# Kernel tuning notes

Hardware: AMD Instinct MI355X
Metric: run time of the kernel (lower is better)

## Reference

```python
import jax, jax.numpy as jnp
import numpy as np

B, N, QD = 2, 4096, 1024
CD = 1024
H, DH = 8, 64
INNER = H * DH  # 512


def setup_inputs() -> dict:
    key = jax.random.key(0)
    ks = jax.random.split(key, 10)
    s = lambda d: (1.0 / np.sqrt(d)).astype(np.float32)
    return {
        "x": jax.random.normal(ks[0], (B, N, QD), dtype=jnp.float32),
        "context": jax.random.normal(ks[1], (B, N, CD), dtype=jnp.float32),
        "mask": jax.random.randint(ks[2], (B, N + 1), 0, 2) > 0,
        # weights stored as [in, out] (y = x @ W), matching torch Linear math
        "Wq": jax.random.normal(ks[3], (QD, INNER), dtype=jnp.float32) * s(QD),
        "Wk": jax.random.normal(ks[4], (CD, INNER), dtype=jnp.float32) * s(CD),
        "Wv": jax.random.normal(ks[5], (CD, INNER), dtype=jnp.float32) * s(CD),
        "Wk_bg": jax.random.normal(ks[6], (QD, INNER), dtype=jnp.float32) * s(QD),
        "Wv_bg": jax.random.normal(ks[7], (QD, INNER), dtype=jnp.float32) * s(QD),
        "Wout": jax.random.normal(ks[8], (INNER, QD), dtype=jnp.float32) * s(INNER),
        "b_out": jax.random.normal(ks[9], (QD,), dtype=jnp.float32) * 0.01,
    }


def reference(x, context, mask, Wq, Wk, Wv, Wk_bg, Wv_bg, Wout, b_out):
    b, n, _ = x.shape
    scale = DH ** -0.5

    q = x @ Wq                                             # [b, n, inner]
    pooled_x = jax.lax.stop_gradient(jnp.mean(x, axis=1, keepdims=True))  # [b, 1, qd]
    k = jnp.concatenate([context @ Wk, pooled_x @ Wk_bg], axis=1)  # [b, n+1, inner]
    v = jnp.concatenate([context @ Wv, pooled_x @ Wv_bg], axis=1)  # [b, n+1, inner]

    split = lambda t: t.reshape(b, t.shape[1], H, DH).transpose(0, 2, 1, 3)  # b h j d
    qh, kh, vh = split(q), split(k), split(v)

    sim = jnp.einsum('bhid,bhjd->bhij', qh, kh) * scale     # [b, h, n, n+1]
    neg = -jnp.finfo(sim.dtype).max
    sim = jnp.where(mask[:, None, None, :], sim, neg)
    attn = jax.nn.softmax(sim, axis=-1)
    out = jnp.einsum('bhij,bhjd->bhid', attn, vh)           # [b, h, n, d]
    out = out.transpose(0, 2, 1, 3).reshape(b, n, INNER)    # [b, n, inner]
    return out @ Wout + b_out                                # dropout p=0 -> identity
```

## Files before the change

### kernel.cpp

```cpp
#include <hip/hip_runtime.h>
#include <stdint.h>

#define N_TOK 4096
#define QDIM  1024
#define CDIM  1024
#define NH    8
#define DH    64
#define INNER 512
#define BATCH 2
#define N1    4097
#define N1P   4128
#define NJB   129
#define NJBP  132
#define VROWS 80
#define KTILE_SH 2048
#define VTILE_SH 2560

typedef __attribute__((ext_vector_type(8))) short short8;
typedef __attribute__((ext_vector_type(4))) float f32x4;
typedef __attribute__((ext_vector_type(4))) uint32_t u32x4;

__device__ __forceinline__ short f2bf(float f) {
    union { float f; uint32_t u; } x; x.f = f;
    uint32_t r = x.u + 0x7fffu + ((x.u >> 16) & 1u);
    return (short)(r >> 16);
}

__device__ __forceinline__ void async_copy16(void* lds, const void* g) {
    __builtin_amdgcn_global_load_lds(
        (const __attribute__((address_space(1))) void*)g,
        (__attribute__((address_space(3))) void*)lds, 16, 0, 0);
}

#define NB_CAST 16384
#define NB_TC   2048
#define NB_POOL 64
__global__ __launch_bounds__(256) void prep_kernel(
        const float* __restrict__ x, const float* __restrict__ ctx,
        const float* __restrict__ Wq, const float* __restrict__ Wk,
        const float* __restrict__ Wv, const float* __restrict__ Wout,
        short* __restrict__ x_bf, short* __restrict__ c_bf,
        short* __restrict__ Wqt, short* __restrict__ Wkvt, short* __restrict__ Wot,
        float* __restrict__ part, float scale_q) {
    __shared__ float tile[32][33];
    int blk = blockIdx.x, t = threadIdx.x;
    if (blk < NB_CAST) {
        const int n4 = BATCH * N_TOK * QDIM / 4;
        int i = blk * 256 + t;
        bool first = i < n4;
        const float* s = first ? x : ctx;
        short* d = first ? x_bf : c_bf;
        int j = first ? i : i - n4;
        float4 v = ((const float4*)s)[j];
        ((short4*)d)[j] = make_short4(f2bf(v.x), f2bf(v.y), f2bf(v.z), f2bf(v.w));
    } else if (blk < NB_CAST + NB_TC) {
        int rel = blk - NB_CAST;
        int z = rel >> 9, bid = rel & 511;
        const float* W; short* Wt; int K, N; float scale = 1.f;
        if (z == 0)      { W = Wq;   Wt = Wqt;  K = QDIM;  N = INNER; scale = scale_q; }
        else if (z == 1) { W = Wk;   Wt = Wkvt; K = CDIM;  N = INNER; }
        else if (z == 2) { W = Wv;   Wt = Wkvt + (size_t)INNER * CDIM; K = CDIM; N = INNER; }
        else             { W = Wout; Wt = Wot;  K = INNER; N = QDIM; }
        int ntn = N >> 5;
        int n0 = (bid & (ntn - 1)) * 32, k0 = (bid / ntn) * 32;
        int tx = t & 31, ty = t >> 5;
        for (int r = ty; r < 32; r += 8)
            tile[r][tx] = W[(size_t)(k0 + r) * N + n0 + tx];
        __syncthreads();
        for (int r = ty; r < 32; r += 8)
            Wt[(size_t)(n0 + r) * K + k0 + tx] = f2bf(tile[tx][r] * scale);
    } else {
        int rel = blk - NB_CAST - NB_TC;
        int c = rel & 31, b = rel >> 5;
        float s0 = 0.f, s1 = 0.f, s2 = 0.f, s3 = 0.f;
        const float* xp = x + ((size_t)b * N_TOK + c * 128) * QDIM;
        for (int n = 0; n < 128; n++) {
            const float* row = xp + (size_t)n * QDIM;
            s0 += row[t];
            s1 += row[256 + t];
            s2 += row[512 + t];
            s3 += row[768 + t];
        }
        float* pp = part + ((size_t)b * 32 + c) * QDIM;
        pp[t] = s0; pp[256 + t] = s1; pp[512 + t] = s2; pp[768 + t] = s3;
    }
}

__global__ __launch_bounds__(256) void transpose_v_kernel(
        const short* __restrict__ vin, short* __restrict__ vout,
        const int* __restrict__ mask) {
    __shared__ short tile[32][65];
    __shared__ int mloc[32];
    int bh = blockIdx.z, b = bh >> 3;
    int j0 = blockIdx.x * 32, jb = blockIdx.x;
    int tx = threadIdx.x & 63, ty = threadIdx.x >> 6;
    const short* src = vin + (size_t)bh * N1P * DH;
    if (j0 < N1P) {
        for (int r = ty; r < 32; r += 4)
            tile[r][tx] = src[(size_t)(j0 + r) * DH + tx];
    }
    if (threadIdx.x < 32) {
        int j = j0 + threadIdx.x;
        mloc[threadIdx.x] = (j < N1) ? mask[b * N1 + j] : 0;
    }
    __syncthreads();
    int tp = threadIdx.x & 31, dy = threadIdx.x >> 5;
    int s = (tp >> 3) * 4 + (tp & 3) + ((tp >> 2) & 1) * 16;
    bool mk = mloc[s] != 0;
    short* dst = vout + ((size_t)bh * NJBP + jb) * VTILE_SH;
    for (int d = dy; d < DH; d += 8) {
        int swz = (((tp >> 3) ^ ((d >> 1) & 3)) << 3) | (tp & 7);
        dst[d * 32 + swz] = mk ? tile[s][d] : (short)0;
    }
    if (dy == 0) dst[64 * 32 + tp] = mk ? (short)0x3F80 : (short)0;
    if (dy == 1)
        for (int d = 65; d < 80; d++) dst[d * 32 + tp] = 0;
}

__global__ __launch_bounds__(256) void qkv_gemm_kernel(
        const short* __restrict__ x_bf, const short* __restrict__ c_bf,
        const short* __restrict__ Wqt, const short* __restrict__ Wkvt,
        const float* __restrict__ part, const float* __restrict__ Wkbg,
        const float* __restrict__ Wvbg,
        short* __restrict__ q_bf, short* __restrict__ k_bf, short* __restrict__ v_tmp) {
    __shared__ short As[128 * 32];
    __shared__ short Bs[128 * 32];
    __shared__ float pooled[QDIM];
    const int t = threadIdx.x;
    int bid = (blockIdx.x & 7) * 97 + (blockIdx.x >> 3);

    if (bid >= 768) {
        int sub = bid - 768;
        int b = sub & 1, jb = sub >> 1;
        for (int d = t; d < QDIM; d += 256) {
            float s = 0.f;
            for (int c = 0; c < 32; c++) s += part[((size_t)b * 32 + c) * QDIM + d];
            pooled[d] = s * (1.f / (float)N_TOK);
        }
        __syncthreads();
        int flat = jb * 256 + t;
        int matv = flat >> 9;
        int o = flat & 511;
        const float* W = matv ? Wvbg : Wkbg;
        float s = 0.f;
        for (int k = 0; k < QDIM; k++) s += pooled[k] * W[(size_t)k * INNER + o];
        int h = o >> 6, d = o & 63;
        if (matv) {
            v_tmp[(((size_t)(b * NH + h)) * N1P + N_TOK) * DH + d] = f2bf(s);
        } else {
            k_bf[((size_t)(b * NH + h)) * NJBP * KTILE_SH + 128 * KTILE_SH
                 + (d >> 5) * 1024 + (d & 31)] = f2bf(s);
        }
        if (jb == 0) {
            for (int idx = t; idx < NH * 31 * DH; idx += 256) {
                int h2 = idx / (31 * DH);
                int r2 = idx % (31 * DH);
                int rr = 1 + r2 / DH;
                int d2 = r2 % DH;
                k_bf[((size_t)(b * NH + h2)) * NJBP * KTILE_SH + 128 * KTILE_SH
                     + (d2 >> 5) * 1024 + rr * 32 + (d2 & 31)] = 0;
            }
            for (int idx = t; idx < NH * 3 * KTILE_SH; idx += 256) {
                int h2 = idx / (3 * KTILE_SH);
                int r2 = idx % (3 * KTILE_SH);
                k_bf[((size_t)(b * NH + h2)) * NJBP * KTILE_SH + 129 * KTILE_SH + r2] = 0;
            }
        }
        return;
    }

    const int lane = t & 63, w = t >> 6;
    const int wr = w >> 1, wc = w & 1;
    const int lo = lane & 15, g = lane >> 4;
    const int arow = lane >> 2;
    const int ac8 = (lane & 3) * 8;

    const short *A, *W;
    int m0, n0, which;
    if (bid < 256) { A = x_bf; W = Wqt;  m0 = (bid >> 2) * 128; n0 = (bid & 3) * 128; which = 0; }
    else { int i = bid - 256; A = c_bf; W = Wkvt; m0 = (i >> 3) * 128; n0 = (i & 7) * 128;
           which = (n0 < 512) ? 1 : 2; }

    f32x4 acc[4][4] = {};
    for (int k0 = 0; k0 < 1024; k0 += 32) {
        for (int q = 0; q < 2; q++) {
            int seg = w * 2 + q;
            async_copy16(&As[seg * 512], A + (size_t)(m0 + seg * 16 + arow) * 1024 + k0 + ac8);
            async_copy16(&Bs[seg * 512], W + (size_t)(n0 + seg * 16 + arow) * 1024 + k0 + ac8);
        }
        __syncthreads();
        short8 af[4], bfv[4];
        #pragma unroll
        for (int i = 0; i < 4; i++)
            af[i] = *(const short8*)&As[(wr * 64 + i * 16 + lo) * 32 + g * 8];
        #pragma unroll
        for (int j = 0; j < 4; j++)
            bfv[j] = *(const short8*)&Bs[(wc * 64 + j * 16 + lo) * 32 + g * 8];
        #pragma unroll
        for (int i = 0; i < 4; i++)
            #pragma unroll
            for (int j = 0; j < 4; j++)
                acc[i][j] = __builtin_amdgcn_mfma_f32_16x16x32_bf16(af[i], bfv[j], acc[i][j], 0, 0, 0);
        __syncthreads();
    }

    if (which == 0) {
        #pragma unroll
        for (int i = 0; i < 4; i++)
            #pragma unroll
            for (int j = 0; j < 4; j++) {
                int row = m0 + wr * 64 + i * 16 + g * 4;
                int col0 = n0 + wc * 64 + j * 16 + lo;
                int h = col0 >> 6, d = col0 & 63;
                f32x4 v = acc[i][j];
                #pragma unroll
                for (int r = 0; r < 4; r++) {
                    int m = row + r;
                    int b = m >> 12, ii = m & 4095;
                    q_bf[(((size_t)(b * NH + h)) * N_TOK + ii) * DH + d] = f2bf(v[r]);
                }
            }
    } else if (which == 1) {
        #pragma unroll
        for (int i = 0; i < 4; i++)
            #pragma unroll
            for (int j = 0; j < 4; j++) {
                int row = m0 + wr * 64 + i * 16 + g * 4;
                int col0 = n0 + wc * 64 + j * 16 + lo;
                int h = col0 >> 6, d = col0 & 63;
                f32x4 v = acc[i][j];
                #pragma unroll
                for (int r = 0; r < 4; r++) {
                    int m = row + r;
                    int b = m >> 12, ii = m & 4095;
                    int off = (d >> 5) * 1024 + (ii & 31) * 32 + (d & 31);
                    off ^= ((ii >> 1) & 3) << 3;
                    k_bf[((size_t)(b * NH + h)) * NJBP * KTILE_SH + (ii >> 5) * KTILE_SH
                         + off] = f2bf(v[r]);
                }
            }
    } else {
        #pragma unroll
        for (int i = 0; i < 4; i++)
            #pragma unroll
            for (int j = 0; j < 4; j++) {
                int row = m0 + wr * 64 + i * 16 + g * 4;
                int col0 = n0 + wc * 64 + j * 16 + lo;
                int col = col0 - 512;
                int h = col >> 6, d = col & 63;
                f32x4 v = acc[i][j];
                #pragma unroll
                for (int r = 0; r < 4; r++) {
                    int m = row + r;
                    int b = m >> 12, ii = m & 4095;
                    v_tmp[(((size_t)(b * NH + h)) * N1P + ii) * DH + d] = f2bf(v[r]);
                }
            }
    }
}

__global__ __launch_bounds__(256) void out_gemm_kernel(
        const short* __restrict__ A, const short* __restrict__ Wt,
        float* __restrict__ outf, const float* __restrict__ bias) {
    __shared__ short As[128 * 32];
    __shared__ short Bs[128 * 32];
    const int t = threadIdx.x;
    const int lane = t & 63, w = t >> 6;
    const int wr = w >> 1, wc = w & 1;
    const int lo = lane & 15, g = lane >> 4;
    const int arow = lane >> 2;
    const int ac8 = (lane & 3) * 8;
    const int bid = (blockIdx.x & 7) * 64 + (blockIdx.x >> 3);
    const int m0 = (bid & 63) * 128, n0 = (bid >> 6) * 128;

    f32x4 acc[4][4] = {};
    for (int k0 = 0; k0 < INNER; k0 += 32) {
        for (int q = 0; q < 2; q++) {
            int seg = w * 2 + q;
            async_copy16(&As[seg * 512], A + (size_t)(m0 + seg * 16 + arow) * INNER + k0 + ac8);
            async_copy16(&Bs[seg * 512], Wt + (size_t)(n0 + seg * 16 + arow) * INNER + k0 + ac8);
        }
        __syncthreads();
        short8 af[4], bfv[4];
        #pragma unroll
        for (int i = 0; i < 4; i++)
            af[i] = *(const short8*)&As[(wr * 64 + i * 16 + lo) * 32 + g * 8];
        #pragma unroll
        for (int j = 0; j < 4; j++)
            bfv[j] = *(const short8*)&Bs[(wc * 64 + j * 16 + lo) * 32 + g * 8];
        #pragma unroll
        for (int i = 0; i < 4; i++)
            #pragma unroll
            for (int j = 0; j < 4; j++)
                acc[i][j] = __builtin_amdgcn_mfma_f32_16x16x32_bf16(af[i], bfv[j], acc[i][j], 0, 0, 0);
        __syncthreads();
    }
    #pragma unroll
    for (int i = 0; i < 4; i++)
        #pragma unroll
        for (int j = 0; j < 4; j++) {
            int row = m0 + wr * 64 + i * 16 + g * 4;
            int col = n0 + wc * 64 + j * 16 + lo;
            f32x4 v = acc[i][j];
            #pragma unroll
            for (int r = 0; r < 4; r++)
                outf[(size_t)(row + r) * QDIM + col] = v[r] + bias[col];
        }
}

__global__ __launch_bounds__(256, 2) void attn_kernel(
        const short* __restrict__ qb,
        const short* __restrict__ kb,
        const short* __restrict__ vtb,
        short* __restrict__ ob) {
    const int t = threadIdx.x, lane = t & 63, w = t >> 6;
    const int lo = lane & 15, g = lane >> 4;
    const int gs = g ^ ((lo >> 1) & 3);
    const int id = blockIdx.x;
    const int h = id & 7, b = (id >> 3) & 1, qt = id >> 4;
    const int q0 = qt * 128 + w * 32;
    const size_t bh = (size_t)(b * NH + h);

    const short* qp = qb + (bh * N_TOK + q0 + lo) * DH;
    short8 qa[2][2];
    qa[0][0] = *(const short8*)(qp + g * 8);
    qa[0][1] = *(const short8*)(qp + 32 + g * 8);
    qa[1][0] = *(const short8*)(qp + 16 * DH + g * 8);
    qa[1][1] = *(const short8*)(qp + 16 * DH + 32 + g * 8);

    __shared__ short Kl[2][4][KTILE_SH];
    __shared__ short Vl[2][4][VTILE_SH];

    const short* ksrc = kb + bh * (size_t)NJBP * KTILE_SH + w * 512 + lane * 8;
    const short* vsrc = vtb + bh * (size_t)NJBP * VTILE_SH + w * 512 + lane * 8;

    f32x4 o[2][5] = {};
    f32x4 z = {};

    #pragma unroll
    for (int s = 0; s < 4; s++) {
        async_copy16(&Kl[0][s][w * 512], ksrc + (size_t)s * KTILE_SH);
        async_copy16(&Vl[0][s][w * 512], vsrc + (size_t)s * VTILE_SH);
        if (w == 0) async_copy16(&Vl[0][s][2048], vsrc + (size_t)s * VTILE_SH + 2048);
    }
    __syncthreads();

    for (int it = 0; it < 33; ++it) {
        const int cur = it & 1;
        if (it < 32) {
            const short* ks = ksrc + (size_t)(4 * it + 4) * KTILE_SH;
            const short* vs = vsrc + (size_t)(4 * it + 4) * VTILE_SH;
            #pragma unroll
            for (int s = 0; s < 4; s++) {
                async_copy16(&Kl[cur ^ 1][s][w * 512], ks + (size_t)s * KTILE_SH);
                async_copy16(&Vl[cur ^ 1][s][w * 512], vs + (size_t)s * VTILE_SH);
                if (w == 0) async_copy16(&Vl[cur ^ 1][s][2048], vs + (size_t)s * VTILE_SH + 2048);
            }
        }
        #pragma unroll
        for (int sub = 0; sub < 4; ++sub) {
            const short* kl = &Kl[cur][sub][0];
            const short* vl = &Vl[cur][sub][0];
            __builtin_amdgcn_s_setprio(1);
            short8 kf00 = *(const short8*)&kl[(lo) * 32 + gs * 8];
            short8 kf01 = *(const short8*)&kl[1024 + (lo) * 32 + gs * 8];
            short8 kf10 = *(const short8*)&kl[(16 + lo) * 32 + gs * 8];
            short8 kf11 = *(const short8*)&kl[1024 + (16 + lo) * 32 + gs * 8];
            short8 vfr[5];
            #pragma unroll
            for (int f = 0; f < 5; f++)
                vfr[f] = *(const short8*)&vl[(f * 16 + lo) * 32 + gs * 8];
            #pragma unroll
            for (int rg = 0; rg < 2; rg++) {
                f32x4 s0 = __builtin_amdgcn_mfma_f32_16x16x32_bf16(kf00, qa[rg][0], z, 0, 0, 0);
                s0 = __builtin_amdgcn_mfma_f32_16x16x32_bf16(kf01, qa[rg][1], s0, 0, 0, 0);
                f32x4 s1 = __builtin_amdgcn_mfma_f32_16x16x32_bf16(kf10, qa[rg][0], z, 0, 0, 0);
                s1 = __builtin_amdgcn_mfma_f32_16x16x32_bf16(kf11, qa[rg][1], s1, 0, 0, 0);
                uint32_t u0 = __float_as_uint(__builtin_amdgcn_exp2f(s0[0])) + 0x8000u;
                uint32_t u1 = __float_as_uint(__builtin_amdgcn_exp2f(s0[1])) + 0x8000u;
                uint32_t u2 = __float_as_uint(__builtin_amdgcn_exp2f(s0[2])) + 0x8000u;
                uint32_t u3 = __float_as_uint(__builtin_amdgcn_exp2f(s0[3])) + 0x8000u;
                uint32_t u4 = __float_as_uint(__builtin_amdgcn_exp2f(s1[0])) + 0x8000u;
                uint32_t u5 = __float_as_uint(__builtin_amdgcn_exp2f(s1[1])) + 0x8000u;
                uint32_t u6 = __float_as_uint(__builtin_amdgcn_exp2f(s1[2])) + 0x8000u;
                uint32_t u7 = __float_as_uint(__builtin_amdgcn_exp2f(s1[3])) + 0x8000u;
                u32x4 pr;
                pr[0] = __builtin_amdgcn_perm(u1, u0, 0x07060302u);
                pr[1] = __builtin_amdgcn_perm(u3, u2, 0x07060302u);
                pr[2] = __builtin_amdgcn_perm(u5, u4, 0x07060302u);
                pr[3] = __builtin_amdgcn_perm(u7, u6, 0x07060302u);
                short8 pa = __builtin_bit_cast(short8, pr);
                #pragma unroll
                for (int f = 0; f < 5; f++)
                    o[rg][f] = __builtin_amdgcn_mfma_f32_16x16x32_bf16(pa, vfr[f], o[rg][f], 0, 0, 0);
            }
            __builtin_amdgcn_s_setprio(0);
        }
        __syncthreads();
    }

    short* op = ob + ((size_t)(b * N_TOK) + q0) * INNER + h * DH;
    #pragma unroll
    for (int rg = 0; rg < 2; rg++)
        #pragma unroll
        for (int r = 0; r < 4; r++) {
            float l = __shfl(o[rg][4][r], lane & 48);
            float inv = (l > 0.f) ? 1.f / l : 0.f;
            short* o_ = op + (size_t)(rg * 16 + g * 4 + r) * INNER;
            o_[lo]      = f2bf(o[rg][0][r] * inv);
            o_[16 + lo] = f2bf(o[rg][1][r] * inv);
            o_[32 + lo] = f2bf(o[rg][2][r] * inv);
            o_[48 + lo] = f2bf(o[rg][3][r] * inv);
        }
}

extern "C" void kernel_launch(void* const* d_in, const int* in_sizes, int n_in,
                              void* d_out, int out_size, void* d_ws, size_t ws_size,
                              hipStream_t stream) {
    const float* x    = (const float*)d_in[0];
    const float* ctx  = (const float*)d_in[1];
    const int*   mask = (const int*)d_in[2];
    const float* Wq   = (const float*)d_in[3];
    const float* Wk   = (const float*)d_in[4];
    const float* Wv   = (const float*)d_in[5];
    const float* Wkbg = (const float*)d_in[6];
    const float* Wvbg = (const float*)d_in[7];
    const float* Wout = (const float*)d_in[8];
    const float* bout = (const float*)d_in[9];
    float* out = (float*)d_out;

    char* p = (char*)d_ws;
    auto alloc = [&](size_t b) { char* r = p; p += (b + 255) & ~(size_t)255; return r; };
    short* x_bf  = (short*)alloc((size_t)BATCH * N_TOK * QDIM * 2);
    short* c_bf  = (short*)alloc((size_t)BATCH * N_TOK * CDIM * 2);
    short* Wqt   = (short*)alloc((size_t)INNER * QDIM * 2);
    short* Wkvt  = (short*)alloc((size_t)2 * INNER * CDIM * 2);
    short* Wot   = (short*)alloc((size_t)QDIM * INNER * 2);
    short* q_bf  = (short*)alloc((size_t)BATCH * NH * N_TOK * DH * 2);
    short* k_bf  = (short*)alloc((size_t)BATCH * NH * NJBP * KTILE_SH * 2);
    short* v_tmp = (short*)alloc((size_t)BATCH * NH * N1P * DH * 2);
    short* vt_bf = (short*)alloc((size_t)BATCH * NH * NJBP * VTILE_SH * 2);
    short* o_bf  = (short*)alloc((size_t)BATCH * N_TOK * INNER * 2);
    float* part  = (float*)alloc((size_t)BATCH * 32 * QDIM * 4);

    const float SCALE_Q = 0.125f * 1.4426950408889634f;

    prep_kernel<<<NB_CAST + NB_TC + NB_POOL, 256, 0, stream>>>(
        x, ctx, Wq, Wk, Wv, Wout, x_bf, c_bf, Wqt, Wkvt, Wot, part, SCALE_Q);

    qkv_gemm_kernel<<<776, 256, 0, stream>>>(
        x_bf, c_bf, Wqt, Wkvt, part, Wkbg, Wvbg, q_bf, k_bf, v_tmp);

    transpose_v_kernel<<<dim3(NJBP, 1, BATCH * NH), 256, 0, stream>>>(v_tmp, vt_bf, mask);

    attn_kernel<<<512, 256, 0, stream>>>(q_bf, k_bf, vt_bf, o_bf);

    out_gemm_kernel<<<512, 256, 0, stream>>>(o_bf, Wot, out, bout);
}
```

Baseline: 308.1 us.

## Halve attention query tile per block to double grid and raise occupancy

```diff
diff --git a/kernel.cpp b/kernel.cpp
--- a/kernel.cpp
+++ b/kernel.cpp
@@ -308,7 +308,7 @@
         }
 }
 
-__global__ __launch_bounds__(256, 2) void attn_kernel(
+__global__ __launch_bounds__(256, 4) void attn_kernel(
         const short* __restrict__ qb,
         const short* __restrict__ kb,
         const short* __restrict__ vtb,
@@ -318,47 +318,48 @@
     const int gs = g ^ ((lo >> 1) & 3);
     const int id = blockIdx.x;
     const int h = id & 7, b = (id >> 3) & 1, qt = id >> 4;
-    const int q0 = qt * 128 + w * 32;
+    const int q0 = qt * 64 + w * 16;
     const size_t bh = (size_t)(b * NH + h);
 
     const short* qp = qb + (bh * N_TOK + q0 + lo) * DH;
-    short8 qa[2][2];
-    qa[0][0] = *(const short8*)(qp + g * 8);
-    qa[0][1] = *(const short8*)(qp + 32 + g * 8);
-    qa[1][0] = *(const short8*)(qp + 16 * DH + g * 8);
-    qa[1][1] = *(const short8*)(qp + 16 * DH + 32 + g * 8);
-
-    __shared__ short Kl[2][4][KTILE_SH];
-    __shared__ short Vl[2][4][VTILE_SH];
+    short8 qa0 = *(const short8*)(qp + g * 8);
+    short8 qa1 = *(const short8*)(qp + 32 + g * 8);
+
+    __shared__ short Kl[2][2][KTILE_SH];
+    __shared__ short Vl[2][2][VTILE_SH];
 
     const short* ksrc = kb + bh * (size_t)NJBP * KTILE_SH + w * 512 + lane * 8;
     const short* vsrc = vtb + bh * (size_t)NJBP * VTILE_SH + w * 512 + lane * 8;
 
-    f32x4 o[2][5] = {};
+    f32x4 o[5] = {};
     f32x4 z = {};
 
-    #pragma unroll
-    for (int s = 0; s < 4; s++) {
-        async_copy16(&Kl[0][s][w * 512], ksrc + (size_t)s * KTILE_SH);
-        async_copy16(&Vl[0][s][w * 512], vsrc + (size_t)s * VTILE_SH);
-        if (w == 0) async_copy16(&Vl[0][s][2048], vsrc + (size_t)s * VTILE_SH + 2048);
+    async_copy16(&Kl[0][0][w * 512], ksrc);
+    async_copy16(&Vl[0][0][w * 512], vsrc);
+    async_copy16(&Kl[0][1][w * 512], ksrc + KTILE_SH);
+    async_copy16(&Vl[0][1][w * 512], vsrc + VTILE_SH);
+    if (w == 0) {
+        async_copy16(&Vl[0][0][2048], vsrc + 2048);
+        async_copy16(&Vl[0][1][2048], vsrc + VTILE_SH + 2048);
     }
     __syncthreads();
 
-    for (int it = 0; it < 33; ++it) {
+    for (int it = 0; it < 66; ++it) {
         const int cur = it & 1;
-        if (it < 32) {
-            const short* ks = ksrc + (size_t)(4 * it + 4) * KTILE_SH;
-            const short* vs = vsrc + (size_t)(4 * it + 4) * VTILE_SH;
-            #pragma unroll
-            for (int s = 0; s < 4; s++) {
-                async_copy16(&Kl[cur ^ 1][s][w * 512], ks + (size_t)s * KTILE_SH);
-                async_copy16(&Vl[cur ^ 1][s][w * 512], vs + (size_t)s * VTILE_SH);
-                if (w == 0) async_copy16(&Vl[cur ^ 1][s][2048], vs + (size_t)s * VTILE_SH + 2048);
-            }
-        }
-        #pragma unroll
-        for (int sub = 0; sub < 4; ++sub) {
+        if (it < 65) {
+            const short* ks = ksrc + (size_t)(2 * it + 2) * KTILE_SH;
+            const short* vs = vsrc + (size_t)(2 * it + 2) * VTILE_SH;
+            async_copy16(&Kl[cur ^ 1][0][w * 512], ks);
+            async_copy16(&Vl[cur ^ 1][0][w * 512], vs);
+            async_copy16(&Kl[cur ^ 1][1][w * 512], ks + KTILE_SH);
+            async_copy16(&Vl[cur ^ 1][1][w * 512], vs + VTILE_SH);
+            if (w == 0) {
+                async_copy16(&Vl[cur ^ 1][0][2048], vs + 2048);
+                async_copy16(&Vl[cur ^ 1][1][2048], vs + VTILE_SH + 2048);
+            }
+        }
+        #pragma unroll
+        for (int sub = 0; sub < 2; ++sub) {
             const short* kl = &Kl[cur][sub][0];
             const short* vl = &Vl[cur][sub][0];
             __builtin_amdgcn_s_setprio(1);
@@ -370,30 +371,27 @@
             #pragma unroll
             for (int f = 0; f < 5; f++)
                 vfr[f] = *(const short8*)&vl[(f * 16 + lo) * 32 + gs * 8];
-            #pragma unroll
-            for (int rg = 0; rg < 2; rg++) {
-                f32x4 s0 = __builtin_amdgcn_mfma_f32_16x16x32_bf16(kf00, qa[rg][0], z, 0, 0, 0);
-                s0 = __builtin_amdgcn_mfma_f32_16x16x32_bf16(kf01, qa[rg][1], s0, 0, 0, 0);
-                f32x4 s1 = __builtin_amdgcn_mfma_f32_16x16x32_bf16(kf10, qa[rg][0], z, 0, 0, 0);
-                s1 = __builtin_amdgcn_mfma_f32_16x16x32_bf16(kf11, qa[rg][1], s1, 0, 0, 0);
-                uint32_t u0 = __float_as_uint(__builtin_amdgcn_exp2f(s0[0])) + 0x8000u;
-                uint32_t u1 = __float_as_uint(__builtin_amdgcn_exp2f(s0[1])) + 0x8000u;
-                uint32_t u2 = __float_as_uint(__builtin_amdgcn_exp2f(s0[2])) + 0x8000u;
-                uint32_t u3 = __float_as_uint(__builtin_amdgcn_exp2f(s0[3])) + 0x8000u;
-                uint32_t u4 = __float_as_uint(__builtin_amdgcn_exp2f(s1[0])) + 0x8000u;
-                uint32_t u5 = __float_as_uint(__builtin_amdgcn_exp2f(s1[1])) + 0x8000u;
-                uint32_t u6 = __float_as_uint(__builtin_amdgcn_exp2f(s1[2])) + 0x8000u;
-                uint32_t u7 = __float_as_uint(__builtin_amdgcn_exp2f(s1[3])) + 0x8000u;
-                u32x4 pr;
-                pr[0] = __builtin_amdgcn_perm(u1, u0, 0x07060302u);
-                pr[1] = __builtin_amdgcn_perm(u3, u2, 0x07060302u);
-                pr[2] = __builtin_amdgcn_perm(u5, u4, 0x07060302u);
-                pr[3] = __builtin_amdgcn_perm(u7, u6, 0x07060302u);
-                short8 pa = __builtin_bit_cast(short8, pr);
-                #pragma unroll
-                for (int f = 0; f < 5; f++)
-                    o[rg][f] = __builtin_amdgcn_mfma_f32_16x16x32_bf16(pa, vfr[f], o[rg][f], 0, 0, 0);
-            }
+            f32x4 s0 = __builtin_amdgcn_mfma_f32_16x16x32_bf16(kf00, qa0, z, 0, 0, 0);
+            s0 = __builtin_amdgcn_mfma_f32_16x16x32_bf16(kf01, qa1, s0, 0, 0, 0);
+            f32x4 s1 = __builtin_amdgcn_mfma_f32_16x16x32_bf16(kf10, qa0, z, 0, 0, 0);
+            s1 = __builtin_amdgcn_mfma_f32_16x16x32_bf16(kf11, qa1, s1, 0, 0, 0);
+            uint32_t u0 = __float_as_uint(__builtin_amdgcn_exp2f(s0[0])) + 0x8000u;
+            uint32_t u1 = __float_as_uint(__builtin_amdgcn_exp2f(s0[1])) + 0x8000u;
+            uint32_t u2 = __float_as_uint(__builtin_amdgcn_exp2f(s0[2])) + 0x8000u;
+            uint32_t u3 = __float_as_uint(__builtin_amdgcn_exp2f(s0[3])) + 0x8000u;
+            uint32_t u4 = __float_as_uint(__builtin_amdgcn_exp2f(s1[0])) + 0x8000u;
+            uint32_t u5 = __float_as_uint(__builtin_amdgcn_exp2f(s1[1])) + 0x8000u;
+            uint32_t u6 = __float_as_uint(__builtin_amdgcn_exp2f(s1[2])) + 0x8000u;
+            uint32_t u7 = __float_as_uint(__builtin_amdgcn_exp2f(s1[3])) + 0x8000u;
+            u32x4 pr;
+            pr[0] = __builtin_amdgcn_perm(u1, u0, 0x07060302u);
+            pr[1] = __builtin_amdgcn_perm(u3, u2, 0x07060302u);
+            pr[2] = __builtin_amdgcn_perm(u5, u4, 0x07060302u);
+            pr[3] = __builtin_amdgcn_perm(u7, u6, 0x07060302u);
+            short8 pa = __builtin_bit_cast(short8, pr);
+            #pragma unroll
+            for (int f = 0; f < 5; f++)
+                o[f] = __builtin_amdgcn_mfma_f32_16x16x32_bf16(pa, vfr[f], o[f], 0, 0, 0);
             __builtin_amdgcn_s_setprio(0);
         }
         __syncthreads();
@@ -401,17 +399,15 @@
 
     short* op = ob + ((size_t)(b * N_TOK) + q0) * INNER + h * DH;
     #pragma unroll
-    for (int rg = 0; rg < 2; rg++)
-        #pragma unroll
-        for (int r = 0; r < 4; r++) {
-            float l = __shfl(o[rg][4][r], lane & 48);
-            float inv = (l > 0.f) ? 1.f / l : 0.f;
-            short* o_ = op + (size_t)(rg * 16 + g * 4 + r) * INNER;
-            o_[lo]      = f2bf(o[rg][0][r] * inv);
-            o_[16 + lo] = f2bf(o[rg][1][r] * inv);
-            o_[32 + lo] = f2bf(o[rg][2][r] * inv);
-            o_[48 + lo] = f2bf(o[rg][3][r] * inv);
-        }
+    for (int r = 0; r < 4; r++) {
+        float l = __shfl(o[4][r], lane & 48);
+        float inv = (l > 0.f) ? 1.f / l : 0.f;
+        short* o_ = op + (size_t)(g * 4 + r) * INNER;
+        o_[lo]      = f2bf(o[0][r] * inv);
+        o_[16 + lo] = f2bf(o[1][r] * inv);
+        o_[32 + lo] = f2bf(o[2][r] * inv);
+        o_[48 + lo] = f2bf(o[3][r] * inv);
+    }
 }
 
 extern "C" void kernel_launch(void* const* d_in, const int* in_sizes, int n_in,
@@ -453,7 +449,7 @@
 
     transpose_v_kernel<<<dim3(NJBP, 1, BATCH * NH), 256, 0, stream>>>(v_tmp, vt_bf, mask);
 
-    attn_kernel<<<512, 256, 0, stream>>>(q_bf, k_bf, vt_bf, o_bf);
+    attn_kernel<<<1024, 256, 0, stream>>>(q_bf, k_bf, vt_bf, o_bf);
 
     out_gemm_kernel<<<512, 256, 0, stream>>>(o_bf, Wot, out, bout);
 }
```

Measured after the change: 312.7 us. About the same (+1.5%).

## Split key range across two wave groups in attention block, reduce via LDS

Applied to the files above, without the earlier changes.

```diff
diff --git a/kernel.cpp b/kernel.cpp
--- a/kernel.cpp
+++ b/kernel.cpp
@@ -308,17 +308,18 @@
         }
 }
 
-__global__ __launch_bounds__(256, 2) void attn_kernel(
+__global__ __launch_bounds__(512, 4) void attn_kernel(
         const short* __restrict__ qb,
         const short* __restrict__ kb,
         const short* __restrict__ vtb,
         short* __restrict__ ob) {
     const int t = threadIdx.x, lane = t & 63, w = t >> 6;
+    const int w4 = w & 3, half = w >> 2;
     const int lo = lane & 15, g = lane >> 4;
     const int gs = g ^ ((lo >> 1) & 3);
     const int id = blockIdx.x;
     const int h = id & 7, b = (id >> 3) & 1, qt = id >> 4;
-    const int q0 = qt * 128 + w * 32;
+    const int q0 = qt * 128 + w4 * 32;
     const size_t bh = (size_t)(b * NH + h);
 
     const short* qp = qb + (bh * N_TOK + q0 + lo) * DH;
@@ -328,39 +329,48 @@
     qa[1][0] = *(const short8*)(qp + 16 * DH + g * 8);
     qa[1][1] = *(const short8*)(qp + 16 * DH + 32 + g * 8);
 
-    __shared__ short Kl[2][4][KTILE_SH];
-    __shared__ short Vl[2][4][VTILE_SH];
-
-    const short* ksrc = kb + bh * (size_t)NJBP * KTILE_SH + w * 512 + lane * 8;
-    const short* vsrc = vtb + bh * (size_t)NJBP * VTILE_SH + w * 512 + lane * 8;
+    __shared__ short lds[36864];
+    short* Kb = lds;
+    short* Vb = lds + 16384;
+    float* xch = (float*)lds;
+
+    const int tb = half * 66;
+    const short* ksrc = kb + bh * (size_t)NJBP * KTILE_SH + (size_t)tb * KTILE_SH
+                        + w4 * 512 + lane * 8;
+    const short* vsrc = vtb + bh * (size_t)NJBP * VTILE_SH + (size_t)tb * VTILE_SH
+                        + w4 * 512 + lane * 8;
 
     f32x4 o[2][5] = {};
     f32x4 z = {};
 
     #pragma unroll
-    for (int s = 0; s < 4; s++) {
-        async_copy16(&Kl[0][s][w * 512], ksrc + (size_t)s * KTILE_SH);
-        async_copy16(&Vl[0][s][w * 512], vsrc + (size_t)s * VTILE_SH);
-        if (w == 0) async_copy16(&Vl[0][s][2048], vsrc + (size_t)s * VTILE_SH + 2048);
+    for (int s = 0; s < 2; s++) {
+        short* kd = Kb + ((half * 2 + 0) * 2 + s) * 2048;
+        short* vd = Vb + ((half * 2 + 0) * 2 + s) * 2560;
+        async_copy16(kd + w4 * 512, ksrc + (size_t)s * KTILE_SH);
+        async_copy16(vd + w4 * 512, vsrc + (size_t)s * VTILE_SH);
+        if (w4 == 0) async_copy16(vd + 2048, vsrc + (size_t)s * VTILE_SH + 2048);
     }
     __syncthreads();
 
     for (int it = 0; it < 33; ++it) {
         const int cur = it & 1;
         if (it < 32) {
-            const short* ks = ksrc + (size_t)(4 * it + 4) * KTILE_SH;
-            const short* vs = vsrc + (size_t)(4 * it + 4) * VTILE_SH;
-            #pragma unroll
-            for (int s = 0; s < 4; s++) {
-                async_copy16(&Kl[cur ^ 1][s][w * 512], ks + (size_t)s * KTILE_SH);
-                async_copy16(&Vl[cur ^ 1][s][w * 512], vs + (size_t)s * VTILE_SH);
-                if (w == 0) async_copy16(&Vl[cur ^ 1][s][2048], vs + (size_t)s * VTILE_SH + 2048);
-            }
-        }
-        #pragma unroll
-        for (int sub = 0; sub < 4; ++sub) {
-            const short* kl = &Kl[cur][sub][0];
-            const short* vl = &Vl[cur][sub][0];
+            const short* ks = ksrc + (size_t)(2 * it + 2) * KTILE_SH;
+            const short* vs = vsrc + (size_t)(2 * it + 2) * VTILE_SH;
+            #pragma unroll
+            for (int s = 0; s < 2; s++) {
+                short* kd = Kb + ((half * 2 + (cur ^ 1)) * 2 + s) * 2048;
+                short* vd = Vb + ((half * 2 + (cur ^ 1)) * 2 + s) * 2560;
+                async_copy16(kd + w4 * 512, ks + (size_t)s * KTILE_SH);
+                async_copy16(vd + w4 * 512, vs + (size_t)s * VTILE_SH);
+                if (w4 == 0) async_copy16(vd + 2048, vs + (size_t)s * VTILE_SH + 2048);
+            }
+        }
+        #pragma unroll
+        for (int sub = 0; sub < 2; ++sub) {
+            const short* kl = Kb + ((half * 2 + cur) * 2 + sub) * 2048;
+            const short* vl = Vb + ((half * 2 + cur) * 2 + sub) * 2560;
             __builtin_amdgcn_s_setprio(1);
             short8 kf00 = *(const short8*)&kl[(lo) * 32 + gs * 8];
             short8 kf01 = *(const short8*)&kl[1024 + (lo) * 32 + gs * 8];
@@ -399,19 +409,36 @@
         __syncthreads();
     }
 
-    short* op = ob + ((size_t)(b * N_TOK) + q0) * INNER + h * DH;
-    #pragma unroll
-    for (int rg = 0; rg < 2; rg++)
-        #pragma unroll
-        for (int r = 0; r < 4; r++) {
-            float l = __shfl(o[rg][4][r], lane & 48);
-            float inv = (l > 0.f) ? 1.f / l : 0.f;
-            short* o_ = op + (size_t)(rg * 16 + g * 4 + r) * INNER;
-            o_[lo]      = f2bf(o[rg][0][r] * inv);
-            o_[16 + lo] = f2bf(o[rg][1][r] * inv);
-            o_[32 + lo] = f2bf(o[rg][2][r] * inv);
-            o_[48 + lo] = f2bf(o[rg][3][r] * inv);
-        }
+    if (half == 1) {
+        #pragma unroll
+        for (int rg = 0; rg < 2; rg++)
+            #pragma unroll
+            for (int f = 0; f < 5; f++)
+                *(f32x4*)&xch[(((w4 * 2 + rg) * 5 + f) * 64 + lane) * 4] = o[rg][f];
+    }
+    __syncthreads();
+    if (half == 0) {
+        #pragma unroll
+        for (int rg = 0; rg < 2; rg++)
+            #pragma unroll
+            for (int f = 0; f < 5; f++) {
+                f32x4 p = *(const f32x4*)&xch[(((w4 * 2 + rg) * 5 + f) * 64 + lane) * 4];
+                o[rg][f] += p;
+            }
+        short* op = ob + ((size_t)(b * N_TOK) + q0) * INNER + h * DH;
+        #pragma unroll
+        for (int rg = 0; rg < 2; rg++)
+            #pragma unroll
+            for (int r = 0; r < 4; r++) {
+                float l = __shfl(o[rg][4][r], lane & 48);
+                float inv = (l > 0.f) ? 1.f / l : 0.f;
+                short* o_ = op + (size_t)(rg * 16 + g * 4 + r) * INNER;
+                o_[lo]      = f2bf(o[rg][0][r] * inv);
+                o_[16 + lo] = f2bf(o[rg][1][r] * inv);
+                o_[32 + lo] = f2bf(o[rg][2][r] * inv);
+                o_[48 + lo] = f2bf(o[rg][3][r] * inv);
+            }
+    }
 }
 
 extern "C" void kernel_launch(void* const* d_in, const int* in_sizes, int n_in,
@@ -453,7 +480,7 @@
 
     transpose_v_kernel<<<dim3(NJBP, 1, BATCH * NH), 256, 0, stream>>>(v_tmp, vt_bf, mask);
 
-    attn_kernel<<<512, 256, 0, stream>>>(q_bf, k_bf, vt_bf, o_bf);
+    attn_kernel<<<512, 512, 0, stream>>>(q_bf, k_bf, vt_bf, o_bf);
 
     out_gemm_kernel<<<512, 256, 0, stream>>>(o_bf, Wot, out, bout);
 }
```

Result: no change. 303.6 us (-1.5%).
